# Optimization experiments

Measured on AMD Instinct MI355X. Metric: run time of the kernel, lower is better.

Reference implementation:

```python
import jax, jax.numpy as jnp
import numpy as np

B, T, C = 4, 2048, 1024
N_HEAD = 16
HEAD_DIM = C // N_HEAD
SCALE = 1.0 / np.sqrt(HEAD_DIM).astype(np.float32)


def setup_inputs() -> dict:
    key = jax.random.key(0)
    ks = jax.random.split(key, 5)
    std = 1.0 / np.sqrt(C).astype(np.float32)
    return {
        "x": jax.random.normal(ks[0], (B, T, C), dtype=jnp.float32),
        "Wq": jax.random.normal(ks[1], (C, C), dtype=jnp.float32) * std,
        "Wk": jax.random.normal(ks[2], (C, C), dtype=jnp.float32) * std,
        "Wv": jax.random.normal(ks[3], (C, C), dtype=jnp.float32) * std,
        "Wo": jax.random.normal(ks[4], (C, C), dtype=jnp.float32) * std,
    }


def reference(x, Wq, Wk, Wv, Wo):
    # nn.Linear(x) == x @ W.T; projections then split heads: (B, H, T, D)
    def split_heads(t):
        return t.reshape(B, T, N_HEAD, HEAD_DIM).transpose(0, 2, 1, 3)

    q = split_heads(x @ Wq.T)
    k = split_heads(x @ Wk.T)
    v = split_heads(x @ Wv.T)

    att = jnp.einsum("bhqd,bhkd->bhqk", q, k) * SCALE  # (B, H, T, T)
    causal = jnp.tril(jnp.ones((T, T), dtype=bool))
    att = jnp.where(causal[None, None], att, -jnp.inf)
    att = jax.nn.softmax(att, axis=-1)
    # dropout = 0.0 (eval): identity
    y = jnp.einsum("bhqk,bhkd->bhqd", att, v)  # (B, H, T, D)
    y = y.transpose(0, 2, 1, 3).reshape(B, T, C)
    return y @ Wo.T
```

## Files before the change

kernel.cpp:

```cpp
#include <hip/hip_runtime.h>
#include <stdint.h>

#define B_SZ   4
#define T_SEQ  2048
#define C_DIM  1024
#define N_HEAD 16
#define HEAD_D 64
#define QSCALE 0.18033688011112042f
#define M_FIX  12.0f

typedef unsigned short u16;
typedef unsigned int   u32;
typedef __bf16  bfv8  __attribute__((ext_vector_type(8)));
typedef float   f32x4 __attribute__((ext_vector_type(4)));

__device__ __forceinline__ u16 f2bf_hu(float f) {
  union { float f; u32 i; } u; u.f = f;
  return (u16)((u.i + 0x8000u) >> 16);
}
__device__ __forceinline__ u32 pkbf16(float a, float b) {
  union { float f; u32 i; } ua, ub; ua.f = a; ub.f = b;
  return ((ua.i + 0x8000u) >> 16) | ((ub.i + 0x8000u) & 0xFFFF0000u);
}
__device__ __forceinline__ float fexp2(float x) {
#if __has_builtin(__builtin_amdgcn_exp2f)
  return __builtin_amdgcn_exp2f(x);
#else
  return __expf(x * 0.69314718f);
#endif
}

__device__ __forceinline__ void async_cp16(const u16* __restrict__ g, u16* l) {
  __builtin_amdgcn_global_load_lds(
      (const __attribute__((address_space(1))) void*)g,
      (__attribute__((address_space(3))) void*)l, 16, 0, 0);
}

__global__ __launch_bounds__(256) void cvt_kernel(const float* __restrict__ src,
                                                  u16* __restrict__ dst, int n4) {
  int i = blockIdx.x * 256 + threadIdx.x;
  if (i < n4) {
    float4 v = ((const float4*)src)[i];
    int2 o; o.x = (int)pkbf16(v.x, v.y); o.y = (int)pkbf16(v.z, v.w);
    ((int2*)dst)[i] = o;
  }
}
__global__ __launch_bounds__(256) void cvt_w_kernel(
    const float* __restrict__ W0, const float* __restrict__ W1,
    const float* __restrict__ W2, const float* __restrict__ W3,
    u16* __restrict__ dst) {
  const float* s = (blockIdx.y == 0) ? W0 : (blockIdx.y == 1) ? W1
                 : (blockIdx.y == 2) ? W2 : W3;
  u16* d = dst + (size_t)blockIdx.y * (C_DIM * C_DIM);
  int i = blockIdx.x * 256 + threadIdx.x;
  float4 v = ((const float4*)s)[i];
  int2 o; o.x = (int)pkbf16(v.x, v.y); o.y = (int)pkbf16(v.z, v.w);
  ((int2*)d)[i] = o;
}

__device__ __forceinline__ void gemm_core(const u16* __restrict__ A,
                                          const u16* __restrict__ Bw,
                                          int m0, int n0,
                                          f32x4 acc[4][4],
                                          u16* As, u16* Bs) {
  const int tid  = threadIdx.x;
  const int wave = tid >> 6;
  const int lane = tid & 63;
  const int frow = lane & 15;
  const int fk   = (lane >> 4) * 8;
  const int wm   = wave >> 1, wn = wave & 1;

  const int lrow = tid >> 2;
  const int lcol = (tid & 3) * 8;
  const u16* ga0 = A  + (size_t)(m0 + lrow)      * C_DIM + lcol;
  const u16* ga1 = A  + (size_t)(m0 + 64 + lrow) * C_DIM + lcol;
  const u16* gb0 = Bw + (size_t)(n0 + lrow)      * C_DIM + lcol;
  const u16* gb1 = Bw + (size_t)(n0 + 64 + lrow) * C_DIM + lcol;
  u16* lA0 = As + tid * 8;
  u16* lA1 = As + 2048 + tid * 8;
  u16* lB0 = Bs + tid * 8;
  u16* lB1 = Bs + 2048 + tid * 8;

  for (int k0 = 0; k0 < C_DIM; k0 += 32) {
    __syncthreads();
    async_cp16(ga0, lA0);
    async_cp16(ga1, lA1);
    async_cp16(gb0, lB0);
    async_cp16(gb1, lB1);
    ga0 += 32; ga1 += 32; gb0 += 32; gb1 += 32;
    __syncthreads();

    bfv8 af[4], bfr[4];
#pragma unroll
    for (int mt = 0; mt < 4; mt++)
      af[mt] = *(const bfv8*)(As + (wm * 64 + mt * 16 + frow) * 32 + fk);
#pragma unroll
    for (int nt = 0; nt < 4; nt++)
      bfr[nt] = *(const bfv8*)(Bs + (wn * 64 + nt * 16 + frow) * 32 + fk);
#pragma unroll
    for (int mt = 0; mt < 4; mt++)
#pragma unroll
      for (int nt = 0; nt < 4; nt++)
        acc[mt][nt] = __builtin_amdgcn_mfma_f32_16x16x32_bf16(
            af[mt], bfr[nt], acc[mt][nt], 0, 0, 0);
  }
}

__global__ __launch_bounds__(256) void gemm_qkv_kernel(
    const u16* __restrict__ X, const u16* __restrict__ Wq,
    const u16* __restrict__ Wk, const u16* __restrict__ Wv,
    u16* __restrict__ Qo, u16* __restrict__ Ko, u16* __restrict__ Vo) {
  __shared__ __align__(16) u16 smem[16384];
  u16* As = smem; u16* Bs = smem + 4096;
  const u16* W = (blockIdx.z == 0) ? Wq : (blockIdx.z == 1) ? Wk : Wv;
  u16* dst     = (blockIdx.z == 0) ? Qo : (blockIdx.z == 1) ? Ko : Vo;
  const int m0 = blockIdx.x * 128, n0 = blockIdx.y * 128;

  f32x4 acc[4][4];
#pragma unroll
  for (int i = 0; i < 4; i++)
#pragma unroll
    for (int j = 0; j < 4; j++) acc[i][j] = {0.f, 0.f, 0.f, 0.f};

  gemm_core(X, W, m0, n0, acc, As, Bs);
  __syncthreads();

  const int lane = threadIdx.x & 63, wave = threadIdx.x >> 6;
  const int wm = wave >> 1, wn = wave & 1;
  const int quad = lane >> 4, col = lane & 15;
  u16* buf = smem + wave * 4096;
  const int bb = (m0 + wm * 64) >> 11;
  const int t0 = (m0 + wm * 64) & (T_SEQ - 1);
  const int h  = (n0 >> 6) + wn;

  if (blockIdx.z == 2) {
#pragma unroll
    for (int mt = 0; mt < 4; mt++)
#pragma unroll
      for (int nt = 0; nt < 4; nt++) {
        int d_l = nt * 16 + col;
        int g   = mt * 4 + quad;
        int gp  = g ^ (d_l & 15);
        int2 o;
        o.x = (int)pkbf16(acc[mt][nt][0], acc[mt][nt][1]);
        o.y = (int)pkbf16(acc[mt][nt][2], acc[mt][nt][3]);
        *(int2*)(buf + d_l * 64 + gp * 4) = o;
      }
#pragma unroll
    for (int tt = 0; tt < 8; tt++) {
      int d_l = tt * 8 + (lane >> 3);
      int seg = lane & 7;
      int g0 = (2 * seg) ^ (d_l & 15), g1 = (2 * seg + 1) ^ (d_l & 15);
      int2 a  = *(const int2*)(buf + d_l * 64 + g0 * 4);
      int2 bv = *(const int2*)(buf + d_l * 64 + g1 * 4);
      int4 o; o.x = a.x; o.y = a.y; o.z = bv.x; o.w = bv.y;
      *(int4*)(Vo + (((size_t)(bb * N_HEAD + h) * HEAD_D + d_l) * T_SEQ
                     + t0 + seg * 8)) = o;
    }
  } else {
    const float sc = (blockIdx.z == 0) ? QSCALE : 1.0f;
#pragma unroll
    for (int mt = 0; mt < 4; mt++)
#pragma unroll
      for (int nt = 0; nt < 4; nt++)
#pragma unroll
        for (int r = 0; r < 4; r++) {
          int m_l = mt * 16 + quad * 4 + r;
          int n_l = nt * 16 + col;
          int gp = (n_l >> 3) ^ (m_l & 7);
          buf[m_l * 64 + gp * 8 + (n_l & 7)] = f2bf_hu(acc[mt][nt][r] * sc);
        }
#pragma unroll
    for (int tt = 0; tt < 8; tt++) {
      int m_l = tt * 8 + (lane >> 3);
      int seg = lane & 7;
      int gp = seg ^ (m_l & 7);
      int4 o = *(const int4*)(buf + m_l * 64 + gp * 8);
      *(int4*)(dst + (((size_t)(bb * N_HEAD + h) * T_SEQ + t0 + m_l) * HEAD_D
                      + seg * 8)) = o;
    }
  }
}

__global__ __launch_bounds__(256) void gemm_out_kernel(
    const u16* __restrict__ Y, const u16* __restrict__ Wo,
    float* __restrict__ Out) {
  __shared__ __align__(16) u16 smem[16384];
  u16* As = smem; u16* Bs = smem + 4096;
  const int m0 = blockIdx.x * 128, n0 = blockIdx.y * 128;

  f32x4 acc[4][4];
#pragma unroll
  for (int i = 0; i < 4; i++)
#pragma unroll
    for (int j = 0; j < 4; j++) acc[i][j] = {0.f, 0.f, 0.f, 0.f};

  gemm_core(Y, Wo, m0, n0, acc, As, Bs);
  __syncthreads();

  const int lane = threadIdx.x & 63, wave = threadIdx.x >> 6;
  const int wm = wave >> 1, wn = wave & 1;
  const int quad = lane >> 4, col = lane & 15;
  float* bufF = (float*)(smem + wave * 4096);

#pragma unroll
  for (int c = 0; c < 2; c++) {
#pragma unroll
    for (int mt = 0; mt < 4; mt++)
#pragma unroll
      for (int nn = 0; nn < 2; nn++)
#pragma unroll
        for (int r = 0; r < 4; r++) {
          int nt = 2 * c + nn;
          int m_l = mt * 16 + quad * 4 + r;
          int n_l = nn * 16 + col;
          int gp = (n_l >> 2) ^ (m_l & 7);
          bufF[m_l * 32 + gp * 4 + (n_l & 3)] = acc[mt][nt][r];
        }
#pragma unroll
    for (int tt = 0; tt < 8; tt++) {
      int m_l = tt * 8 + (lane >> 3);
      int seg = lane & 7;
      int gp = seg ^ (m_l & 7);
      float4 o = *(const float4*)(bufF + m_l * 32 + gp * 4);
      *(float4*)(Out + (size_t)(m0 + wm * 64 + m_l) * C_DIM
                 + n0 + wn * 64 + c * 32 + seg * 4) = o;
    }
  }
}

#define ATT_Q 128

__global__ __launch_bounds__(256, 4) void attn_kernel(
    const u16* __restrict__ Qg, const u16* __restrict__ Kg,
    const u16* __restrict__ Vtg, u16* __restrict__ Yg) {
  __shared__ __align__(16) u16 QPs[128 * 64];
  __shared__ __align__(16) u16 Ks[64 * 64];
  __shared__ __align__(16) u16 Vt[64 * 64];

  const int tid = threadIdx.x;
  const int wave = tid >> 6, lane = tid & 63;
  const int quad = lane >> 4, l15 = lane & 15;
  const int bh = blockIdx.x;
  const int b = bh >> 4, h = bh & 15;
  const int yy = blockIdx.y, gq = yy >> 2, rq = yy & 3;
  const int qt = (gq == 0) ? 15 - rq : (gq == 1) ? rq
               : (gq == 2) ? 11 - rq : 4 + rq;
  const int q0 = qt * ATT_Q;

  {
    const int row = tid >> 1;
    const int c0 = (tid & 1) * 32;
    const u16* gp = Qg + ((size_t)bh * T_SEQ + q0 + row) * HEAD_D + c0;
#pragma unroll
    for (int g = 0; g < 4; g++) {
      int4 v = *(const int4*)(gp + g * 8);
      int pg = ((c0 >> 3) + g) ^ (row & 7);
      *(int4*)(QPs + row * 64 + pg * 8) = v;
    }
  }
  __syncthreads();

  bfv8 qb[2][2];
#pragma unroll
  for (int nt = 0; nt < 2; nt++)
#pragma unroll
    for (int ks = 0; ks < 2; ks++) {
      int q = wave * 32 + nt * 16 + l15;
      int pg = (ks * 4 + quad) ^ (q & 7);
      qb[nt][ks] = *(const bfv8*)(QPs + q * 64 + pg * 8);
    }

  float l_i[2] = {0.f, 0.f};
  f32x4 ao[4][2];
#pragma unroll
  for (int mt = 0; mt < 4; mt++)
#pragma unroll
    for (int nt = 0; nt < 2; nt++) ao[mt][nt] = {0.f, 0.f, 0.f, 0.f};

  const int srow = tid >> 2;
  const int sc0 = (tid & 3) * 16;
  const u16* gkb = Kg  + (size_t)bh * T_SEQ * HEAD_D + (size_t)srow * HEAD_D + sc0;
  const u16* gvb = Vtg + (size_t)bh * HEAD_D * T_SEQ + (size_t)srow * T_SEQ + sc0;
  const int pg0 = (sc0 >> 3) ^ (srow & 7), pg1 = ((sc0 >> 3) + 1) ^ (srow & 7);

  int4 kr0, kr1, vr0, vr1;
  kr0 = *(const int4*)(gkb);      kr1 = *(const int4*)(gkb + 8);
  vr0 = *(const int4*)(gvb);      vr1 = *(const int4*)(gvb + 8);

  const int ktmax = 2 * qt + 1;
  for (int kt = 0; kt <= ktmax; kt++) {
    __syncthreads();
    *(int4*)(Ks + srow * 64 + pg0 * 8) = kr0;
    *(int4*)(Ks + srow * 64 + pg1 * 8) = kr1;
    *(int4*)(Vt + srow * 64 + pg0 * 8) = vr0;
    *(int4*)(Vt + srow * 64 + pg1 * 8) = vr1;
    __syncthreads();
    if (kt < ktmax) {
      const u16* gk = gkb + (size_t)(kt + 1) * 64 * HEAD_D;
      const u16* gv = gvb + (kt + 1) * 64;
      kr0 = *(const int4*)(gk);  kr1 = *(const int4*)(gk + 8);
      vr0 = *(const int4*)(gv);  vr1 = *(const int4*)(gv + 8);
    }

    f32x4 as[4][2];
#pragma unroll
    for (int mt = 0; mt < 4; mt++)
#pragma unroll
      for (int nt = 0; nt < 2; nt++) as[mt][nt] = {0.f, 0.f, 0.f, 0.f};
#pragma unroll
    for (int mt = 0; mt < 4; mt++) {
      bfv8 ka[2];
#pragma unroll
      for (int ks = 0; ks < 2; ks++) {
        int key = mt * 16 + l15;
        int pg = (ks * 4 + quad) ^ (key & 7);
        ka[ks] = *(const bfv8*)(Ks + key * 64 + pg * 8);
      }
#pragma unroll
      for (int nt = 0; nt < 2; nt++)
#pragma unroll
        for (int ks = 0; ks < 2; ks++)
          as[mt][nt] = __builtin_amdgcn_mfma_f32_16x16x32_bf16(
              ka[ks], qb[nt][ks], as[mt][nt], 0, 0, 0);
    }

    const bool diag = (kt >= 2 * qt);
#pragma unroll
    for (int nt = 0; nt < 2; nt++) {
      const int q_l = wave * 32 + nt * 16 + l15;
      const int q_g = q0 + q_l;
      float lacc = 0.f;
#pragma unroll
      for (int mt = 0; mt < 4; mt++) {
        float p[4];
#pragma unroll
        for (int r = 0; r < 4; r++) {
          float s = as[mt][nt][r];
          if (diag) {
            int key_g = kt * 64 + mt * 16 + quad * 4 + r;
            if (key_g > q_g) s = -1e30f;
          }
          p[r] = fexp2(s - M_FIX);
        }
        lacc += (p[0] + p[1]) + (p[2] + p[3]);
        int pg = (2 * mt + (quad >> 1)) ^ (q_l & 7);
        int2 o;
        o.x = (int)pkbf16(p[0], p[1]);
        o.y = (int)pkbf16(p[2], p[3]);
        *(int2*)(QPs + q_l * 64 + pg * 8 + (quad & 1) * 4) = o;
      }
      l_i[nt] += lacc;
    }

    bfv8 pf[2][2];
#pragma unroll
    for (int nt = 0; nt < 2; nt++)
#pragma unroll
      for (int ks = 0; ks < 2; ks++) {
        int q_l = wave * 32 + nt * 16 + l15;
        int pg = (ks * 4 + quad) ^ (q_l & 7);
        pf[nt][ks] = *(const bfv8*)(QPs + q_l * 64 + pg * 8);
      }
#pragma unroll
    for (int mt = 0; mt < 4; mt++) {
      bfv8 va[2];
#pragma unroll
      for (int ks = 0; ks < 2; ks++) {
        int d = mt * 16 + l15;
        int pg = (ks * 4 + quad) ^ (d & 7);
        va[ks] = *(const bfv8*)(Vt + d * 64 + pg * 8);
      }
#pragma unroll
      for (int nt = 0; nt < 2; nt++)
#pragma unroll
        for (int ks = 0; ks < 2; ks++)
          ao[mt][nt] = __builtin_amdgcn_mfma_f32_16x16x32_bf16(
              va[ks], pf[nt][ks], ao[mt][nt], 0, 0, 0);
    }
  }

#pragma unroll
  for (int nt = 0; nt < 2; nt++) {
    l_i[nt] += __shfl_xor(l_i[nt], 16);
    l_i[nt] += __shfl_xor(l_i[nt], 32);
  }

  __syncthreads();
#pragma unroll
  for (int nt = 0; nt < 2; nt++) {
    float inv = 1.0f / l_i[nt];
    int q_l = wave * 32 + nt * 16 + l15;
#pragma unroll
    for (int mt = 0; mt < 4; mt++) {
      int g = mt * 4 + quad;
      int gp = g ^ (q_l & 15);
      int2 o;
      o.x = (int)pkbf16(ao[mt][nt][0] * inv, ao[mt][nt][1] * inv);
      o.y = (int)pkbf16(ao[mt][nt][2] * inv, ao[mt][nt][3] * inv);
      *(int2*)(QPs + q_l * 64 + gp * 4) = o;
    }
  }
  __syncthreads();
#pragma unroll
  for (int rr = 0; rr < 4; rr++) {
    int q   = rr * 32 + (tid >> 3);
    int seg = tid & 7;
    int g0 = (2 * seg) ^ (q & 15), g1 = (2 * seg + 1) ^ (q & 15);
    int2 a  = *(const int2*)(QPs + q * 64 + g0 * 4);
    int2 bv = *(const int2*)(QPs + q * 64 + g1 * 4);
    int4 o; o.x = a.x; o.y = a.y; o.z = bv.x; o.w = bv.y;
    *(int4*)(Yg + ((size_t)b * T_SEQ + q0 + q) * C_DIM + h * HEAD_D + seg * 8) = o;
  }
}

extern "C" void kernel_launch(void* const* d_in, const int* in_sizes, int n_in,
                              void* d_out, int out_size, void* d_ws, size_t ws_size,
                              hipStream_t stream) {
  const float* x  = (const float*)d_in[0];
  const float* Wq = (const float*)d_in[1];
  const float* Wk = (const float*)d_in[2];
  const float* Wv = (const float*)d_in[3];
  const float* Wo = (const float*)d_in[4];
  float* out = (float*)d_out;

  const size_t NE = (size_t)B_SZ * T_SEQ * C_DIM;
  const size_t NW = (size_t)C_DIM * C_DIM;
  u16* xbf = (u16*)d_ws;
  u16* wqb = xbf + NE;
  u16* wkb = wqb + NW;
  u16* wvb = wkb + NW;
  u16* wob = wvb + NW;
  u16* qws = wob + NW;
  u16* kws = qws + NE;
  u16* vws = kws + NE;
  u16* yws = vws + NE;

  cvt_kernel<<<(int)(NE / 4 / 256), 256, 0, stream>>>(x, xbf, (int)(NE / 4));
  cvt_w_kernel<<<dim3((int)(NW / 4 / 256), 4), 256, 0, stream>>>(Wq, Wk, Wv, Wo, wqb);

  dim3 g1(T_SEQ * B_SZ / 128, C_DIM / 128, 3);
  gemm_qkv_kernel<<<g1, 256, 0, stream>>>(xbf, wqb, wkb, wvb, qws, kws, vws);

  dim3 g2(B_SZ * N_HEAD, T_SEQ / ATT_Q);
  attn_kernel<<<g2, 256, 0, stream>>>(qws, kws, vws, yws);

  dim3 g3(T_SEQ * B_SZ / 128, C_DIM / 128);
  gemm_out_kernel<<<g3, 256, 0, stream>>>(yws, wob, out);
}
```

Baseline: 254.8 us.

## Double-buffer LDS tiles in the GEMM core to overlap loads with MFMA

```diff
diff --git a/kernel.cpp b/kernel.cpp
--- a/kernel.cpp
+++ b/kernel.cpp
@@ -58,11 +58,30 @@
   ((int2*)d)[i] = o;
 }
 
+__device__ __forceinline__ void mfma_step(const u16* Sbuf, int wm, int wn,
+                                          int frow, int fk, f32x4 acc[4][4]) {
+  const u16* As = Sbuf;
+  const u16* Bs = Sbuf + 4096;
+  bfv8 af[4], bfr[4];
+#pragma unroll
+  for (int mt = 0; mt < 4; mt++)
+    af[mt] = *(const bfv8*)(As + (wm * 64 + mt * 16 + frow) * 32 + fk);
+#pragma unroll
+  for (int nt = 0; nt < 4; nt++)
+    bfr[nt] = *(const bfv8*)(Bs + (wn * 64 + nt * 16 + frow) * 32 + fk);
+#pragma unroll
+  for (int mt = 0; mt < 4; mt++)
+#pragma unroll
+    for (int nt = 0; nt < 4; nt++)
+      acc[mt][nt] = __builtin_amdgcn_mfma_f32_16x16x32_bf16(
+          af[mt], bfr[nt], acc[mt][nt], 0, 0, 0);
+}
+
 __device__ __forceinline__ void gemm_core(const u16* __restrict__ A,
                                           const u16* __restrict__ Bw,
                                           int m0, int n0,
                                           f32x4 acc[4][4],
-                                          u16* As, u16* Bs) {
+                                          u16* smem) {
   const int tid  = threadIdx.x;
   const int wave = tid >> 6;
   const int lane = tid & 63;
@@ -76,34 +95,30 @@
   const u16* ga1 = A  + (size_t)(m0 + 64 + lrow) * C_DIM + lcol;
   const u16* gb0 = Bw + (size_t)(n0 + lrow)      * C_DIM + lcol;
   const u16* gb1 = Bw + (size_t)(n0 + 64 + lrow) * C_DIM + lcol;
-  u16* lA0 = As + tid * 8;
-  u16* lA1 = As + 2048 + tid * 8;
-  u16* lB0 = Bs + tid * 8;
-  u16* lB1 = Bs + 2048 + tid * 8;
-
-  for (int k0 = 0; k0 < C_DIM; k0 += 32) {
+  u16* b0 = smem;
+  u16* b1 = smem + 8192;
+  const int so = tid * 8;
+
+#define STAGE_TO(dst) do {                        \
+    async_cp16(ga0, (dst) + so);                  \
+    async_cp16(ga1, (dst) + 2048 + so);           \
+    async_cp16(gb0, (dst) + 4096 + so);           \
+    async_cp16(gb1, (dst) + 6144 + so);           \
+    ga0 += 32; ga1 += 32; gb0 += 32; gb1 += 32;   \
+  } while (0)
+
+  STAGE_TO(b0);
+  __syncthreads();
+
+  for (int it = 0; it < 32; it += 2) {
+    STAGE_TO(b1);
+    mfma_step(b0, wm, wn, frow, fk, acc);
     __syncthreads();
-    async_cp16(ga0, lA0);
-    async_cp16(ga1, lA1);
-    async_cp16(gb0, lB0);
-    async_cp16(gb1, lB1);
-    ga0 += 32; ga1 += 32; gb0 += 32; gb1 += 32;
+    if (it < 30) STAGE_TO(b0);
+    mfma_step(b1, wm, wn, frow, fk, acc);
     __syncthreads();
-
-    bfv8 af[4], bfr[4];
-#pragma unroll
-    for (int mt = 0; mt < 4; mt++)
-      af[mt] = *(const bfv8*)(As + (wm * 64 + mt * 16 + frow) * 32 + fk);
-#pragma unroll
-    for (int nt = 0; nt < 4; nt++)
-      bfr[nt] = *(const bfv8*)(Bs + (wn * 64 + nt * 16 + frow) * 32 + fk);
-#pragma unroll
-    for (int mt = 0; mt < 4; mt++)
-#pragma unroll
-      for (int nt = 0; nt < 4; nt++)
-        acc[mt][nt] = __builtin_amdgcn_mfma_f32_16x16x32_bf16(
-            af[mt], bfr[nt], acc[mt][nt], 0, 0, 0);
-  }
+  }
+#undef STAGE_TO
 }
 
 __global__ __launch_bounds__(256) void gemm_qkv_kernel(
@@ -111,7 +126,6 @@
     const u16* __restrict__ Wk, const u16* __restrict__ Wv,
     u16* __restrict__ Qo, u16* __restrict__ Ko, u16* __restrict__ Vo) {
   __shared__ __align__(16) u16 smem[16384];
-  u16* As = smem; u16* Bs = smem + 4096;
   const u16* W = (blockIdx.z == 0) ? Wq : (blockIdx.z == 1) ? Wk : Wv;
   u16* dst     = (blockIdx.z == 0) ? Qo : (blockIdx.z == 1) ? Ko : Vo;
   const int m0 = blockIdx.x * 128, n0 = blockIdx.y * 128;
@@ -122,7 +136,7 @@
 #pragma unroll
     for (int j = 0; j < 4; j++) acc[i][j] = {0.f, 0.f, 0.f, 0.f};
 
-  gemm_core(X, W, m0, n0, acc, As, Bs);
+  gemm_core(X, W, m0, n0, acc, smem);
   __syncthreads();
 
   const int lane = threadIdx.x & 63, wave = threadIdx.x >> 6;
@@ -186,7 +200,6 @@
     const u16* __restrict__ Y, const u16* __restrict__ Wo,
     float* __restrict__ Out) {
   __shared__ __align__(16) u16 smem[16384];
-  u16* As = smem; u16* Bs = smem + 4096;
   const int m0 = blockIdx.x * 128, n0 = blockIdx.y * 128;
 
   f32x4 acc[4][4];
@@ -195,7 +208,7 @@
 #pragma unroll
     for (int j = 0; j < 4; j++) acc[i][j] = {0.f, 0.f, 0.f, 0.f};
 
-  gemm_core(Y, Wo, m0, n0, acc, As, Bs);
+  gemm_core(Y, Wo, m0, n0, acc, smem);
   __syncthreads();
 
   const int lane = threadIdx.x & 63, wave = threadIdx.x >> 6;
```

After: 246.6 us. 1.03x faster.
